# Optimization experiments

Hardware: AMD Instinct MI355X
Metric: run time of the kernel (lower is better)

The kernel has to match this reference:

```python
import jax, jax.numpy as jnp
import numpy as np

IN_F = 1024
HID_F = 4096
OUT_F = 1024
B = 64
D = 768
SPARSE_RATIO = 0.1


def setup_inputs() -> dict:
    key = jax.random.key(0)
    k_x, k_w1, k_w2, k_b, k_m = jax.random.split(key, 5)
    # x: [batch, tokens(d), in_features(s)]
    x = jax.random.normal(k_x, (B, D, IN_F), dtype=jnp.float32)
    # scale weights like typical init so GELU inputs stay in a sane range
    fc1_w = jax.random.normal(k_w1, (HID_F, IN_F), dtype=jnp.float32) * (1.0 / np.sqrt(IN_F))
    fc2_w = jax.random.normal(k_w2, (OUT_F, HID_F), dtype=jnp.float32) * (1.0 / np.sqrt(HID_F))
    fc2_b = jax.random.normal(k_b, (OUT_F,), dtype=jnp.float32) * 0.02
    sparse_mask = (jax.random.uniform(k_m, (IN_F, OUT_F)) < SPARSE_RATIO).astype(jnp.float32)
    return {"x": x, "fc1_w": fc1_w, "fc2_w": fc2_w, "fc2_b": fc2_b, "sparse_mask": sparse_mask}


def reference(x, fc1_w, fc2_w, fc2_b, sparse_mask):
    # attn_s[s,t] = sum_d fc1_w[d,s] * fc2_w[t,d] + fc2_b[t]   -> [in, out]
    attn = (jnp.einsum('ds,td->st', fc1_w, fc2_w) + fc2_b) * sparse_mask
    # dropout with p=0.0 is the identity
    out = jnp.einsum('bds,st->bdt', x, attn)  # [B, D, out]
    # torch nn.GELU default is the exact (erf) variant
    return jax.nn.gelu(out, approximate=False)
```

## Files before the change

kernel.cpp:

```cpp
#include <hip/hip_runtime.h>
#include <hip/hip_bf16.h>
#include <math.h>

typedef __attribute__((ext_vector_type(8))) short  short8;
typedef __attribute__((ext_vector_type(4))) float  floatx4;

__device__ __forceinline__ ushort f2bf(float f) {
    __hip_bfloat16 hb = __float2bfloat16(f);
    return *(ushort*)&hb;
}
__device__ __forceinline__ short8 pack8(float4 a, float4 b) {
    union { short8 v; ushort u[8]; } r;
    r.u[0] = f2bf(a.x); r.u[1] = f2bf(a.y); r.u[2] = f2bf(a.z); r.u[3] = f2bf(a.w);
    r.u[4] = f2bf(b.x); r.u[5] = f2bf(b.y); r.u[6] = f2bf(b.z); r.u[7] = f2bf(b.w);
    return r.v;
}

__global__ __launch_bounds__(256) void k_cvt(const float* __restrict__ in,
                                             ushort* __restrict__ out, int n8) {
    int i = blockIdx.x * 256 + threadIdx.x;
    if (i >= n8) return;
    const float4* p = reinterpret_cast<const float4*>(in) + (size_t)i * 2;
    float4 a = p[0], b = p[1];
    *reinterpret_cast<short8*>(out + (size_t)i * 8) = pack8(a, b);
}

__global__ __launch_bounds__(256) void k_transpose(const float* __restrict__ in,
                                                   ushort* __restrict__ out) {
    __shared__ float sm[64][65];
    const int tid = threadIdx.x;
    const int s0 = blockIdx.x * 64;
    const int d0 = blockIdx.y * 64;
#pragma unroll
    for (int i = 0; i < 4; ++i) {
        int lin = i * 256 + tid;
        int dr  = lin >> 4;
        int sc4 = lin & 15;
        float4 v = *reinterpret_cast<const float4*>(&in[(size_t)(d0 + dr) * 1024 + s0 + sc4 * 4]);
        sm[dr][sc4 * 4 + 0] = v.x; sm[dr][sc4 * 4 + 1] = v.y;
        sm[dr][sc4 * 4 + 2] = v.z; sm[dr][sc4 * 4 + 3] = v.w;
    }
    __syncthreads();
#pragma unroll
    for (int i = 0; i < 8; ++i) {
        int lin = i * 256 + tid;
        int dc2 = lin & 31;
        int sr  = lin >> 5;
        uint lo = (uint)f2bf(sm[dc2 * 2][sr]);
        uint hi = (uint)f2bf(sm[dc2 * 2 + 1][sr]);
        *reinterpret_cast<uint*>(&out[(size_t)(s0 + sr) * 4096 + d0 + dc2 * 2]) = lo | (hi << 16);
    }
}

template <int AFP32, int EPI>
__global__ __launch_bounds__(256) void k_gemm(const void* __restrict__ Ap,
                                              const ushort* __restrict__ B,
                                              const float* __restrict__ bias,
                                              const float* __restrict__ mask,
                                              void* __restrict__ Cout,
                                              int lda, int ldb, int ksteps) {
    __shared__ ushort As[128 * 32];
    __shared__ ushort Bs[128 * 32];
    const int tid  = threadIdx.x;
    const int wave = tid >> 6, lane = tid & 63;
    const int wm = wave >> 1, wn = wave & 1;
    const int quad = lane >> 4, m16 = lane & 15;
    const int n0 = blockIdx.x * 128;
    const int m0 = blockIdx.y * 128;

    floatx4 acc[4][4];
    const floatx4 zero = {0.f, 0.f, 0.f, 0.f};
#pragma unroll
    for (int i = 0; i < 4; ++i)
#pragma unroll
        for (int j = 0; j < 4; ++j) acc[i][j] = zero;

    const int s_r = tid >> 2;
    const int s_c = tid & 3;

    for (int kt = 0; kt < ksteps; ++kt) {
        const int k0 = kt * 32;
        short8 a0, a1, b0, b1;
        if (AFP32) {
            const float* Af = (const float*)Ap;
            const float* r0 = &Af[(size_t)(m0 + s_r) * lda + k0 + s_c * 8];
            const float* r1 = &Af[(size_t)(m0 + 64 + s_r) * lda + k0 + s_c * 8];
            a0 = pack8(*reinterpret_cast<const float4*>(r0), *reinterpret_cast<const float4*>(r0 + 4));
            a1 = pack8(*reinterpret_cast<const float4*>(r1), *reinterpret_cast<const float4*>(r1 + 4));
        } else {
            const ushort* Ab = (const ushort*)Ap;
            a0 = *reinterpret_cast<const short8*>(&Ab[(size_t)(m0 + s_r) * lda + k0 + s_c * 8]);
            a1 = *reinterpret_cast<const short8*>(&Ab[(size_t)(m0 + 64 + s_r) * lda + k0 + s_c * 8]);
        }
        b0 = *reinterpret_cast<const short8*>(&B[(size_t)(n0 + s_r) * ldb + k0 + s_c * 8]);
        b1 = *reinterpret_cast<const short8*>(&B[(size_t)(n0 + 64 + s_r) * ldb + k0 + s_c * 8]);
        __syncthreads();
        *reinterpret_cast<short8*>(&As[(s_r)      * 32 + s_c * 8]) = a0;
        *reinterpret_cast<short8*>(&As[(64 + s_r) * 32 + s_c * 8]) = a1;
        *reinterpret_cast<short8*>(&Bs[(s_r)      * 32 + s_c * 8]) = b0;
        *reinterpret_cast<short8*>(&Bs[(64 + s_r) * 32 + s_c * 8]) = b1;
        __syncthreads();

        short8 aF[4], bF[4];
#pragma unroll
        for (int i = 0; i < 4; ++i)
            aF[i] = *reinterpret_cast<const short8*>(&As[(wm * 64 + i * 16 + m16) * 32 + quad * 8]);
#pragma unroll
        for (int j = 0; j < 4; ++j)
            bF[j] = *reinterpret_cast<const short8*>(&Bs[(wn * 64 + j * 16 + m16) * 32 + quad * 8]);
#pragma unroll
        for (int i = 0; i < 4; ++i)
#pragma unroll
            for (int j = 0; j < 4; ++j)
                acc[i][j] = __builtin_amdgcn_mfma_f32_16x16x32_bf16(aF[i], bF[j], acc[i][j], 0, 0, 0);
    }

#pragma unroll
    for (int i = 0; i < 4; ++i) {
#pragma unroll
        for (int j = 0; j < 4; ++j) {
            const int col = n0 + wn * 64 + j * 16 + m16;
            float bv = 0.f;
            if (EPI == 0) bv = bias[col];
#pragma unroll
            for (int rr = 0; rr < 4; ++rr) {
                const int row = m0 + wm * 64 + i * 16 + quad * 4 + rr;
                float v = acc[i][j][rr];
                if (EPI == 0) {
                    v = (v + bv) * mask[(size_t)row * 1024 + col];
                    ((ushort*)Cout)[(size_t)col * 1024 + row] = f2bf(v);
                } else {
                    float g = 0.5f * v * (1.0f + erff(v * 0.70710678118654752f));
                    ((float*)Cout)[(size_t)row * 1024 + col] = g;
                }
            }
        }
    }
}

extern "C" void kernel_launch(void* const* d_in, const int* in_sizes, int n_in,
                              void* d_out, int out_size, void* d_ws, size_t ws_size,
                              hipStream_t stream) {
    const float* x    = (const float*)d_in[0];
    const float* fc1w = (const float*)d_in[1];
    const float* fc2w = (const float*)d_in[2];
    const float* fc2b = (const float*)d_in[3];
    const float* mask = (const float*)d_in[4];

    char* ws = (char*)d_ws;
    ushort* fc1T  = (ushort*)ws;
    ushort* fc2wb = (ushort*)(ws + (8u  << 20));
    ushort* attnT = (ushort*)(ws + (16u << 20));
    ushort* xb    = (ushort*)(ws + (18u << 20));
    const size_t XB_BYTES = 50331648ull * 2;
    const bool has_xb = ws_size >= (size_t)(18u << 20) + XB_BYTES;

    k_transpose<<<dim3(16, 64), 256, 0, stream>>>(fc1w, fc1T);
    k_cvt<<<2048, 256, 0, stream>>>(fc2w, fc2wb, 524288);
    k_gemm<0, 0><<<dim3(8, 8), 256, 0, stream>>>(fc1T, fc2wb, fc2b, mask, attnT,
                                                 4096, 4096, 128);
    if (has_xb) {
        k_cvt<<<24576, 256, 0, stream>>>(x, xb, 6291456);
        k_gemm<0, 1><<<dim3(8, 384), 256, 0, stream>>>(xb, attnT, nullptr, nullptr,
                                                       d_out, 1024, 1024, 32);
    } else {
        k_gemm<1, 1><<<dim3(8, 384), 256, 0, stream>>>(x, attnT, nullptr, nullptr,
                                                       d_out, 1024, 1024, 32);
    }
}
```

Baseline: 612.5 us.

## Use direct global-to-LDS loads, XCD-aware block swizzle, and smaller tiles for attn GEMM

Staging of A and B tiles now goes through the global_load_lds builtin, which copies straight from global memory into shared memory instead of through registers. It also adds a block-index remap that groups consecutive workgroups by modulo 8, aimed at L2 locality across XCDs. The first GEMM moves to 64x64 tiles on a 16x16 grid to occupy more CUs. The data path is unchanged, but the single-buffered loop still synchronizes twice per k-step, and the swizzle assumes the block count divides evenly by 8.

```diff
diff --git a/kernel.cpp b/kernel.cpp
--- a/kernel.cpp
+++ b/kernel.cpp
@@ -14,6 +14,12 @@
     r.u[0] = f2bf(a.x); r.u[1] = f2bf(a.y); r.u[2] = f2bf(a.z); r.u[3] = f2bf(a.w);
     r.u[4] = f2bf(b.x); r.u[5] = f2bf(b.y); r.u[6] = f2bf(b.z); r.u[7] = f2bf(b.w);
     return r.v;
+}
+
+typedef __attribute__((address_space(1))) const void* gas1_t;
+typedef __attribute__((address_space(3))) void*       las3_t;
+__device__ __forceinline__ void gload16(const void* g, void* l) {
+    __builtin_amdgcn_global_load_lds((gas1_t)g, (las3_t)l, 16, 0, 0);
 }
 
 __global__ __launch_bounds__(256) void k_cvt(const float* __restrict__ in,
@@ -52,79 +58,83 @@
     }
 }
 
-template <int AFP32, int EPI>
-__global__ __launch_bounds__(256) void k_gemm(const void* __restrict__ Ap,
-                                              const ushort* __restrict__ B,
-                                              const float* __restrict__ bias,
-                                              const float* __restrict__ mask,
-                                              void* __restrict__ Cout,
-                                              int lda, int ldb, int ksteps) {
-    __shared__ ushort As[128 * 32];
-    __shared__ ushort Bs[128 * 32];
+template <int BM, int BN, int EPI, int SWZ>
+__global__ __launch_bounds__(256) void k_gemm_b(const ushort* __restrict__ A,
+                                                const ushort* __restrict__ B,
+                                                const float* __restrict__ bias,
+                                                const float* __restrict__ mask,
+                                                void* __restrict__ Cout,
+                                                int lda, int ldb, int ksteps) {
+    __shared__ ushort As[BM * 32];
+    __shared__ ushort Bs[BN * 32];
     const int tid  = threadIdx.x;
     const int wave = tid >> 6, lane = tid & 63;
     const int wm = wave >> 1, wn = wave & 1;
     const int quad = lane >> 4, m16 = lane & 15;
-    const int n0 = blockIdx.x * 128;
-    const int m0 = blockIdx.y * 128;
-
-    floatx4 acc[4][4];
+
+    int bx = blockIdx.x, by = blockIdx.y;
+    if (SWZ) {
+        const int nx   = gridDim.x;
+        const int nwg  = nx * gridDim.y;
+        const int orig = by * nx + bx;
+        const int cpx  = nwg >> 3;
+        const int w    = (orig & 7) * cpx + (orig >> 3);
+        bx = w % nx; by = w / nx;
+    }
+    const int n0 = bx * BN;
+    const int m0 = by * BM;
+
+    constexpr int AI = BM / 32;
+    constexpr int BJ = BN / 32;
+    floatx4 acc[AI][BJ];
     const floatx4 zero = {0.f, 0.f, 0.f, 0.f};
 #pragma unroll
-    for (int i = 0; i < 4; ++i)
-#pragma unroll
-        for (int j = 0; j < 4; ++j) acc[i][j] = zero;
-
-    const int s_r = tid >> 2;
-    const int s_c = tid & 3;
+    for (int i = 0; i < AI; ++i)
+#pragma unroll
+        for (int j = 0; j < BJ; ++j) acc[i][j] = zero;
+
+    const int gr = lane >> 2;
+    const int gc = (lane & 3) * 8;
 
     for (int kt = 0; kt < ksteps; ++kt) {
         const int k0 = kt * 32;
-        short8 a0, a1, b0, b1;
-        if (AFP32) {
-            const float* Af = (const float*)Ap;
-            const float* r0 = &Af[(size_t)(m0 + s_r) * lda + k0 + s_c * 8];
-            const float* r1 = &Af[(size_t)(m0 + 64 + s_r) * lda + k0 + s_c * 8];
-            a0 = pack8(*reinterpret_cast<const float4*>(r0), *reinterpret_cast<const float4*>(r0 + 4));
-            a1 = pack8(*reinterpret_cast<const float4*>(r1), *reinterpret_cast<const float4*>(r1 + 4));
-        } else {
-            const ushort* Ab = (const ushort*)Ap;
-            a0 = *reinterpret_cast<const short8*>(&Ab[(size_t)(m0 + s_r) * lda + k0 + s_c * 8]);
-            a1 = *reinterpret_cast<const short8*>(&Ab[(size_t)(m0 + 64 + s_r) * lda + k0 + s_c * 8]);
-        }
-        b0 = *reinterpret_cast<const short8*>(&B[(size_t)(n0 + s_r) * ldb + k0 + s_c * 8]);
-        b1 = *reinterpret_cast<const short8*>(&B[(size_t)(n0 + 64 + s_r) * ldb + k0 + s_c * 8]);
+        if (kt) __syncthreads();
+#pragma unroll
+        for (int t = 0; t < BM / 64; ++t) {
+            const int r = wave * (BM / 4) + t * 16;
+            gload16(&A[(size_t)(m0 + r + gr) * lda + k0 + gc], &As[r * 32]);
+        }
+#pragma unroll
+        for (int t = 0; t < BN / 64; ++t) {
+            const int r = wave * (BN / 4) + t * 16;
+            gload16(&B[(size_t)(n0 + r + gr) * ldb + k0 + gc], &Bs[r * 32]);
+        }
         __syncthreads();
-        *reinterpret_cast<short8*>(&As[(s_r)      * 32 + s_c * 8]) = a0;
-        *reinterpret_cast<short8*>(&As[(64 + s_r) * 32 + s_c * 8]) = a1;
-        *reinterpret_cast<short8*>(&Bs[(s_r)      * 32 + s_c * 8]) = b0;
-        *reinterpret_cast<short8*>(&Bs[(64 + s_r) * 32 + s_c * 8]) = b1;
-        __syncthreads();
-
-        short8 aF[4], bF[4];
-#pragma unroll
-        for (int i = 0; i < 4; ++i)
-            aF[i] = *reinterpret_cast<const short8*>(&As[(wm * 64 + i * 16 + m16) * 32 + quad * 8]);
-#pragma unroll
-        for (int j = 0; j < 4; ++j)
-            bF[j] = *reinterpret_cast<const short8*>(&Bs[(wn * 64 + j * 16 + m16) * 32 + quad * 8]);
-#pragma unroll
-        for (int i = 0; i < 4; ++i)
-#pragma unroll
-            for (int j = 0; j < 4; ++j)
+
+        short8 aF[AI], bF[BJ];
+#pragma unroll
+        for (int i = 0; i < AI; ++i)
+            aF[i] = *reinterpret_cast<const short8*>(&As[(wm * (BM / 2) + i * 16 + m16) * 32 + quad * 8]);
+#pragma unroll
+        for (int j = 0; j < BJ; ++j)
+            bF[j] = *reinterpret_cast<const short8*>(&Bs[(wn * (BN / 2) + j * 16 + m16) * 32 + quad * 8]);
+#pragma unroll
+        for (int i = 0; i < AI; ++i)
+#pragma unroll
+            for (int j = 0; j < BJ; ++j)
                 acc[i][j] = __builtin_amdgcn_mfma_f32_16x16x32_bf16(aF[i], bF[j], acc[i][j], 0, 0, 0);
     }
 
 #pragma unroll
-    for (int i = 0; i < 4; ++i) {
-#pragma unroll
-        for (int j = 0; j < 4; ++j) {
-            const int col = n0 + wn * 64 + j * 16 + m16;
+    for (int i = 0; i < AI; ++i) {
+#pragma unroll
+        for (int j = 0; j < BJ; ++j) {
+            const int col = n0 + wn * (BN / 2) + j * 16 + m16;
             float bv = 0.f;
             if (EPI == 0) bv = bias[col];
 #pragma unroll
             for (int rr = 0; rr < 4; ++rr) {
-                const int row = m0 + wm * 64 + i * 16 + quad * 4 + rr;
+                const int row = m0 + wm * (BM / 2) + i * 16 + quad * 4 + rr;
                 float v = acc[i][j][rr];
                 if (EPI == 0) {
                     v = (v + bv) * mask[(size_t)row * 1024 + col];
@@ -138,6 +148,75 @@
     }
 }
 
+__global__ __launch_bounds__(256) void k_gemm_f32a(const float* __restrict__ Af,
+                                                   const ushort* __restrict__ B,
+                                                   float* __restrict__ Cout,
+                                                   int lda, int ldb, int ksteps) {
+    __shared__ ushort As[128 * 32];
+    __shared__ ushort Bs[128 * 32];
+    const int tid  = threadIdx.x;
+    const int wave = tid >> 6, lane = tid & 63;
+    const int wm = wave >> 1, wn = wave & 1;
+    const int quad = lane >> 4, m16 = lane & 15;
+    const int n0 = blockIdx.x * 128;
+    const int m0 = blockIdx.y * 128;
+
+    floatx4 acc[4][4];
+    const floatx4 zero = {0.f, 0.f, 0.f, 0.f};
+#pragma unroll
+    for (int i = 0; i < 4; ++i)
+#pragma unroll
+        for (int j = 0; j < 4; ++j) acc[i][j] = zero;
+
+    const int s_r = tid >> 2;
+    const int s_c = tid & 3;
+    const int gr = lane >> 2;
+    const int gc = (lane & 3) * 8;
+
+    for (int kt = 0; kt < ksteps; ++kt) {
+        const int k0 = kt * 32;
+        const float* r0 = &Af[(size_t)(m0 + s_r) * lda + k0 + s_c * 8];
+        const float* r1 = &Af[(size_t)(m0 + 64 + s_r) * lda + k0 + s_c * 8];
+        short8 a0 = pack8(*reinterpret_cast<const float4*>(r0), *reinterpret_cast<const float4*>(r0 + 4));
+        short8 a1 = pack8(*reinterpret_cast<const float4*>(r1), *reinterpret_cast<const float4*>(r1 + 4));
+        __syncthreads();
+        *reinterpret_cast<short8*>(&As[(s_r)      * 32 + s_c * 8]) = a0;
+        *reinterpret_cast<short8*>(&As[(64 + s_r) * 32 + s_c * 8]) = a1;
+#pragma unroll
+        for (int t = 0; t < 2; ++t) {
+            const int r = wave * 32 + t * 16;
+            gload16(&B[(size_t)(n0 + r + gr) * ldb + k0 + gc], &Bs[r * 32]);
+        }
+        __syncthreads();
+
+        short8 aF[4], bF[4];
+#pragma unroll
+        for (int i = 0; i < 4; ++i)
+            aF[i] = *reinterpret_cast<const short8*>(&As[(wm * 64 + i * 16 + m16) * 32 + quad * 8]);
+#pragma unroll
+        for (int j = 0; j < 4; ++j)
+            bF[j] = *reinterpret_cast<const short8*>(&Bs[(wn * 64 + j * 16 + m16) * 32 + quad * 8]);
+#pragma unroll
+        for (int i = 0; i < 4; ++i)
+#pragma unroll
+            for (int j = 0; j < 4; ++j)
+                acc[i][j] = __builtin_amdgcn_mfma_f32_16x16x32_bf16(aF[i], bF[j], acc[i][j], 0, 0, 0);
+    }
+
+#pragma unroll
+    for (int i = 0; i < 4; ++i)
+#pragma unroll
+        for (int j = 0; j < 4; ++j) {
+            const int col = n0 + wn * 64 + j * 16 + m16;
+#pragma unroll
+            for (int rr = 0; rr < 4; ++rr) {
+                const int row = m0 + wm * 64 + i * 16 + quad * 4 + rr;
+                float v = acc[i][j][rr];
+                Cout[(size_t)row * 1024 + col] = 0.5f * v * (1.0f + erff(v * 0.70710678118654752f));
+            }
+        }
+}
+
 extern "C" void kernel_launch(void* const* d_in, const int* in_sizes, int n_in,
                               void* d_out, int out_size, void* d_ws, size_t ws_size,
                               hipStream_t stream) {
@@ -157,14 +236,13 @@
 
     k_transpose<<<dim3(16, 64), 256, 0, stream>>>(fc1w, fc1T);
     k_cvt<<<2048, 256, 0, stream>>>(fc2w, fc2wb, 524288);
-    k_gemm<0, 0><<<dim3(8, 8), 256, 0, stream>>>(fc1T, fc2wb, fc2b, mask, attnT,
-                                                 4096, 4096, 128);
+    k_gemm_b<64, 64, 0, 1><<<dim3(16, 16), 256, 0, stream>>>(
+        fc1T, fc2wb, fc2b, mask, attnT, 4096, 4096, 128);
     if (has_xb) {
         k_cvt<<<24576, 256, 0, stream>>>(x, xb, 6291456);
-        k_gemm<0, 1><<<dim3(8, 384), 256, 0, stream>>>(xb, attnT, nullptr, nullptr,
-                                                       d_out, 1024, 1024, 32);
+        k_gemm_b<128, 128, 1, 1><<<dim3(8, 384), 256, 0, stream>>>(
+            xb, attnT, nullptr, nullptr, d_out, 1024, 1024, 32);
     } else {
-        k_gemm<1, 1><<<dim3(8, 384), 256, 0, stream>>>(x, attnT, nullptr, nullptr,
-                                                       d_out, 1024, 1024, 32);
-    }
-}
+        k_gemm_f32a<<<dim3(8, 384), 256, 0, stream>>>(x, attnT, (float*)d_out, 1024, 1024, 32);
+    }
+}
```

Result: faster. 559.9 us (-8.6%).
